# Performance work log

Measured on AMD Instinct MI355X. Metric: run time of the kernel, lower is better.

Reference implementation:

```python
import jax, jax.numpy as jnp
import numpy as np

HEAD_DIM = 64
MASK_PENALTY = 1000000.0


def setup_inputs() -> dict:
    key = jax.random.key(0)
    kq, kk, kv, ki = jax.random.split(key, 4)
    B, H, S, D = 32, 16, 512, HEAD_DIM
    E, CAP = 8, 4  # n_experts = hidden(1024)//128, capacity per expert
    Q = jax.random.normal(kq, (B, H, S, D), dtype=jnp.float32)
    K = jax.random.normal(kk, (B, H, S, D), dtype=jnp.float32)
    V = jax.random.normal(kv, (B, H, S, D), dtype=jnp.float32)
    idx_list = jax.random.randint(ki, (E, CAP), 0, B)  # per-expert routed batch indices
    mask = jnp.ones((B, S), dtype=jnp.float32)
    return {"Q": Q, "K": K, "V": V, "idx_list": idx_list, "mask": mask}


def reference(Q, K, V, idx_list, mask):
    # Per-expert grouped attention: gather routed batch rows, QK^T, masked
    # softmax, AV. Dropout is identity in eval mode.
    scale = 1.0 / jnp.sqrt(jnp.asarray(HEAD_DIM, dtype=Q.dtype))

    def expert_attn(idx_e):
        q = Q[idx_e]            # [cap, H, S, D]
        k = K[idx_e]
        v = V[idx_e]
        m = mask[idx_e]         # [cap, S]
        dot = jnp.einsum('bhsd,bhtd->bhst', q, k) * scale
        dot = dot - MASK_PENALTY * (1.0 - m[:, None, None, :])
        p = jax.nn.softmax(dot, axis=-1)
        return jnp.einsum('bhst,bhtd->bhsd', p, v)  # [cap, H, S, D]

    X = jax.vmap(expert_attn)(idx_list)  # [E, cap, H, S, D]
    return X
```

## Files before the change

### kernel.cpp

```cpp
#include <hip/hip_runtime.h>
#include <math.h>


typedef _Float16 f16x8 __attribute__((ext_vector_type(8)));
typedef _Float16 f16x2 __attribute__((ext_vector_type(2)));
typedef float    f32x4 __attribute__((ext_vector_type(4)));

#define MFMA16(a, b, c) __builtin_amdgcn_mfma_f32_16x16x32_f16((a), (b), (c), 0, 0, 0)

constexpr int Hh = 16;
constexpr int Ss = 512;
constexpr int Dd = 64;
constexpr int QB = 256;
constexpr int KVB = 64;
constexpr int NT = Ss / KVB;
constexpr float QS = 0.125f * 1.44269504088896f;
constexpr float BM = 1000000.0f * 1.44269504088896f;

union U8 { f16x8 v; f16x2 h[4]; };

__device__ __forceinline__ int SW(int row, int col) {
  return row * 64 + (col ^ ((row & 7) << 3));
}

__device__ __forceinline__ f16x2 pkrtz(float a, float b) {
  auto t = __builtin_amdgcn_cvt_pkrtz(a, b);
  return *(f16x2*)&t;
}

__global__ __launch_bounds__(512) void sparse_attn_kernel(
    const float* __restrict__ Q, const float* __restrict__ K,
    const float* __restrict__ V, const int* __restrict__ idx,
    const float* __restrict__ mask, float* __restrict__ out) {
  const int tid  = threadIdx.x;
  const int lane = tid & 63;
  const int wv   = tid >> 6;
  const int r    = lane & 15;
  const int g    = lane >> 4;

  const int phys = blockIdx.x;
  const int G    = (phys & 7) | ((phys >> 4) << 3);
  const int qb   = (phys >> 3) & 1;
  const int h    = G & 15;
  const int ec   = G >> 4;
  const int b    = idx[ec];

  __shared__ _Float16 Ks[64 * 64];
  __shared__ _Float16 VTs[64 * 64];
  __shared__ float    biasS[Ss];

  const size_t bh = ((size_t)b * Hh + h) * (size_t)Ss * Dd;
  const float* Qb = Q + bh;
  const float* Kb = K + bh;
  const float* Vb = V + bh;
  const float* mrow = mask + (size_t)b * Ss;

  biasS[tid] = mrow[tid] * BM - BM;

  const int q0 = qb * QB + wv * 32;

  f16x8 qf[2][2];
#pragma unroll
  for (int mi = 0; mi < 2; ++mi)
#pragma unroll
    for (int kk = 0; kk < 2; ++kk) {
      const float* qp = Qb + (size_t)(q0 + mi * 16 + r) * Dd + kk * 32 + g * 8;
      float4 x0 = *(const float4*)qp;
      float4 x1 = *(const float4*)(qp + 4);
      U8 u;
      u.h[0] = pkrtz(x0.x * QS, x0.y * QS);
      u.h[1] = pkrtz(x0.z * QS, x0.w * QS);
      u.h[2] = pkrtz(x1.x * QS, x1.y * QS);
      u.h[3] = pkrtz(x1.z * QS, x1.w * QS);
      qf[mi][kk] = u.v;
    }

  f16x8 ones;
#pragma unroll
  for (int e = 0; e < 8; ++e) ones[e] = (_Float16)1.0f;

  f32x4 oacc[2][4];
#pragma unroll
  for (int mi = 0; mi < 2; ++mi)
#pragma unroll
    for (int nj = 0; nj < 4; ++nj) oacc[mi][nj] = (f32x4){0.f, 0.f, 0.f, 0.f};
  f32x4 lacc[2] = {(f32x4){0.f, 0.f, 0.f, 0.f}, (f32x4){0.f, 0.f, 0.f, 0.f}};

  float4 kx0, kx1;
  float  vv[8];

#define K_ISSUE(KV0)                                                         \
  {                                                                          \
    const float* kp_ = Kb + (size_t)((KV0) + (tid >> 3)) * Dd + (tid & 7) * 8;\
    kx0 = *(const float4*)kp_;                                               \
    kx1 = *(const float4*)(kp_ + 4);                                         \
  }

#define V_ISSUE(KV0)                                                         \
  {                                                                          \
    int oct = tid >> 6;                                                      \
    int kb1 = (oct >> 2) * 16 + (oct & 3) * 4;                               \
    const float* vp = Vb + (size_t)((KV0) + kb1) * Dd + (tid & 63);          \
    _Pragma("unroll")                                                        \
    for (int jj = 0; jj < 4; ++jj) {                                         \
      vv[jj]     = vp[(size_t)jj * Dd];                                      \
      vv[jj + 4] = vp[(size_t)(jj + 32) * Dd];                               \
    }                                                                        \
  }

#define STAGE_K()                                                            \
  {                                                                          \
    U8 u;                                                                    \
    u.h[0] = pkrtz(kx0.x, kx0.y);                                            \
    u.h[1] = pkrtz(kx0.z, kx0.w);                                            \
    u.h[2] = pkrtz(kx1.x, kx1.y);                                            \
    u.h[3] = pkrtz(kx1.z, kx1.w);                                            \
    *(f16x8*)&Ks[SW(tid >> 3, (tid & 7) * 8)] = u.v;                         \
  }

#define STAGE_V()                                                            \
  {                                                                          \
    U8 u2;                                                                   \
    u2.h[0] = pkrtz(vv[0], vv[1]);                                           \
    u2.h[1] = pkrtz(vv[2], vv[3]);                                           \
    u2.h[2] = pkrtz(vv[4], vv[5]);                                           \
    u2.h[3] = pkrtz(vv[6], vv[7]);                                           \
    *(f16x8*)&VTs[SW(tid & 63, (tid >> 6) * 8)] = u2.v;                      \
  }

  K_ISSUE(0)
  V_ISSUE(0)
  STAGE_K()
  K_ISSUE(KVB)
  __syncthreads();

  for (int t = 0; t < NT; ++t) {
    const int kv0 = t * KVB;

    STAGE_V()
    if (t < NT - 1) V_ISSUE(kv0 + KVB)

    f32x4 sf[2][4];
#pragma unroll
    for (int nj = 0; nj < 4; ++nj) {
      f32x4 bv = *(const f32x4*)&biasS[kv0 + nj * 16 + g * 4];
      sf[0][nj] = bv; sf[1][nj] = bv;
    }
    __builtin_amdgcn_s_setprio(1);
#pragma unroll
    for (int nj = 0; nj < 4; ++nj)
#pragma unroll
      for (int kk = 0; kk < 2; ++kk) {
        f16x8 kf = *(const f16x8*)&Ks[SW(nj * 16 + r, kk * 32 + g * 8)];
        sf[0][nj] = MFMA16(kf, qf[0][kk], sf[0][nj]);
        sf[1][nj] = MFMA16(kf, qf[1][kk], sf[1][nj]);
      }
    __builtin_amdgcn_s_setprio(0);
    __syncthreads();

    f16x8 pf[2][2];
#pragma unroll
    for (int mi = 0; mi < 2; ++mi) {
      float p[4][4];
#pragma unroll
      for (int nj = 0; nj < 4; ++nj)
#pragma unroll
        for (int rg = 0; rg < 4; ++rg)
          p[nj][rg] = __builtin_amdgcn_exp2f(sf[mi][nj][rg]);
#pragma unroll
      for (int kk = 0; kk < 2; ++kk) {
        U8 u;
        u.h[0] = pkrtz(p[kk][0], p[kk][1]);
        u.h[1] = pkrtz(p[kk][2], p[kk][3]);
        u.h[2] = pkrtz(p[kk + 2][0], p[kk + 2][1]);
        u.h[3] = pkrtz(p[kk + 2][2], p[kk + 2][3]);
        pf[mi][kk] = u.v;
      }
    }

    __builtin_amdgcn_s_setprio(1);
#pragma unroll
    for (int kk = 0; kk < 2; ++kk) {
      lacc[0] = MFMA16(pf[0][kk], ones, lacc[0]);
      lacc[1] = MFMA16(pf[1][kk], ones, lacc[1]);
#pragma unroll
      for (int nj = 0; nj < 4; ++nj) {
        f16x8 vf = *(const f16x8*)&VTs[SW(nj * 16 + r, kk * 32 + g * 8)];
        oacc[0][nj] = MFMA16(pf[0][kk], vf, oacc[0][nj]);
        oacc[1][nj] = MFMA16(pf[1][kk], vf, oacc[1][nj]);
      }
    }
    __builtin_amdgcn_s_setprio(0);

    if (t < NT - 1) {
      STAGE_K()
      if (t < NT - 2) K_ISSUE(kv0 + 2 * KVB)
      __syncthreads();
    }
  }

  float* ob = out + ((size_t)ec * Hh + h) * (size_t)Ss * Dd;
#pragma unroll
  for (int mi = 0; mi < 2; ++mi) {
    float i4[4];
#pragma unroll
    for (int rg = 0; rg < 4; ++rg) i4[rg] = 1.0f / lacc[mi][rg];
#pragma unroll
    for (int nj = 0; nj < 4; ++nj)
#pragma unroll
      for (int rg = 0; rg < 4; ++rg) {
        int row = q0 + mi * 16 + g * 4 + rg;
        int dim = nj * 16 + r;
        ob[(size_t)row * Dd + dim] = oacc[mi][nj][rg] * i4[rg];
      }
  }
}

extern "C" void kernel_launch(void* const* d_in, const int* in_sizes, int n_in,
                              void* d_out, int out_size, void* d_ws, size_t ws_size,
                              hipStream_t stream) {
  const float* Q    = (const float*)d_in[0];
  const float* K    = (const float*)d_in[1];
  const float* V    = (const float*)d_in[2];
  const int*   idx  = (const int*)d_in[3];
  const float* mask = (const float*)d_in[4];
  float* out = (float*)d_out;
  dim3 grid(1024), block(512);
  hipLaunchKernelGGL(sparse_attn_kernel, grid, block, 0, stream,
                     Q, K, V, idx, mask, out);
}
```

Baseline: 60.21 us.

## Double-buffer K and V tiles in LDS to remove one barrier per iteration

Both the K and V shared-memory tiles are now double-buffered. Each iteration stages the next tile's K and V into the alternate buffer and issues global loads two tiles ahead. The mid-iteration barrier between QK and PV is removed, leaving one sync per tile. LDS use doubles and more registers stay live across the loop, which may lower occupancy.

Result: slower. 62.86 us (+4.4%).

```diff
diff --git a/kernel.cpp b/kernel.cpp
--- a/kernel.cpp
+++ b/kernel.cpp
@@ -45,8 +45,8 @@
   const int ec   = G >> 4;
   const int b    = idx[ec];
 
-  __shared__ _Float16 Ks[64 * 64];
-  __shared__ _Float16 VTs[64 * 64];
+  __shared__ _Float16 Ks[2][64 * 64];
+  __shared__ _Float16 VTs[2][64 * 64];
   __shared__ float    biasS[Ss];
 
   const size_t bh = ((size_t)b * Hh + h) * (size_t)Ss * Dd;
@@ -108,37 +108,46 @@
     }                                                                        \
   }
 
-#define STAGE_K()                                                            \
+#define STAGE_K(B)                                                           \
   {                                                                          \
     U8 u;                                                                    \
     u.h[0] = pkrtz(kx0.x, kx0.y);                                            \
     u.h[1] = pkrtz(kx0.z, kx0.w);                                            \
     u.h[2] = pkrtz(kx1.x, kx1.y);                                            \
     u.h[3] = pkrtz(kx1.z, kx1.w);                                            \
-    *(f16x8*)&Ks[SW(tid >> 3, (tid & 7) * 8)] = u.v;                         \
-  }
-
-#define STAGE_V()                                                            \
+    *(f16x8*)&Ks[B][SW(tid >> 3, (tid & 7) * 8)] = u.v;                      \
+  }
+
+#define STAGE_V(B)                                                           \
   {                                                                          \
     U8 u2;                                                                   \
     u2.h[0] = pkrtz(vv[0], vv[1]);                                           \
     u2.h[1] = pkrtz(vv[2], vv[3]);                                           \
     u2.h[2] = pkrtz(vv[4], vv[5]);                                           \
     u2.h[3] = pkrtz(vv[6], vv[7]);                                           \
-    *(f16x8*)&VTs[SW(tid & 63, (tid >> 6) * 8)] = u2.v;                      \
+    *(f16x8*)&VTs[B][SW(tid & 63, (tid >> 6) * 8)] = u2.v;                   \
   }
 
   K_ISSUE(0)
   V_ISSUE(0)
-  STAGE_K()
+  STAGE_K(0)
+  STAGE_V(0)
   K_ISSUE(KVB)
+  V_ISSUE(KVB)
   __syncthreads();
 
+  int cur = 0;
   for (int t = 0; t < NT; ++t) {
     const int kv0 = t * KVB;
 
-    STAGE_V()
-    if (t < NT - 1) V_ISSUE(kv0 + KVB)
+    if (t < NT - 1) {
+      STAGE_K(cur ^ 1)
+      STAGE_V(cur ^ 1)
+      if (t < NT - 2) {
+        K_ISSUE(kv0 + 2 * KVB)
+        V_ISSUE(kv0 + 2 * KVB)
+      }
+    }
 
     f32x4 sf[2][4];
 #pragma unroll
@@ -151,12 +160,11 @@
     for (int nj = 0; nj < 4; ++nj)
 #pragma unroll
       for (int kk = 0; kk < 2; ++kk) {
-        f16x8 kf = *(const f16x8*)&Ks[SW(nj * 16 + r, kk * 32 + g * 8)];
+        f16x8 kf = *(const f16x8*)&Ks[cur][SW(nj * 16 + r, kk * 32 + g * 8)];
         sf[0][nj] = MFMA16(kf, qf[0][kk], sf[0][nj]);
         sf[1][nj] = MFMA16(kf, qf[1][kk], sf[1][nj]);
       }
     __builtin_amdgcn_s_setprio(0);
-    __syncthreads();
 
     f16x8 pf[2][2];
 #pragma unroll
@@ -185,18 +193,15 @@
       lacc[1] = MFMA16(pf[1][kk], ones, lacc[1]);
 #pragma unroll
       for (int nj = 0; nj < 4; ++nj) {
-        f16x8 vf = *(const f16x8*)&VTs[SW(nj * 16 + r, kk * 32 + g * 8)];
+        f16x8 vf = *(const f16x8*)&VTs[cur][SW(nj * 16 + r, kk * 32 + g * 8)];
         oacc[0][nj] = MFMA16(pf[0][kk], vf, oacc[0][nj]);
         oacc[1][nj] = MFMA16(pf[1][kk], vf, oacc[1][nj]);
       }
     }
     __builtin_amdgcn_s_setprio(0);
 
-    if (t < NT - 1) {
-      STAGE_K()
-      if (t < NT - 2) K_ISSUE(kv0 + 2 * KVB)
-      __syncthreads();
-    }
+    if (t < NT - 1) __syncthreads();
+    cur ^= 1;
   }
 
   float* ob = out + ((size_t)ec * Hh + h) * (size_t)Ss * Dd;
```
